# Optimization experiments

Measured on AMD Instinct MI355X. Metric: run time of the kernel, lower is better.

Reference implementation:

```python
import jax, jax.numpy as jnp
import numpy as np

H = 8   # num_heads
D = 64  # out_features per head

def setup_inputs() -> dict:
    key = jax.random.key(0)
    k1, k2, k3, k4 = jax.random.split(key, 4)
    B, N, F_IN, E = 2, 8192, 512, 65536
    x = jax.random.normal(k1, (B, N, F_IN), dtype=jnp.float32)
    edge_indices = jax.random.randint(k2, (2, E), 0, N)
    W = jax.random.normal(k3, (H * D, F_IN), dtype=jnp.float32) * (1.0 / np.sqrt(F_IN))
    a = jax.random.normal(k4, (2 * D, 1), dtype=jnp.float32) * 0.1
    return {"x": x, "edge_indices": edge_indices, "W": W, "a": a}

def reference(x, edge_indices, W, a):
    # Faithful translation of GraphAttentionLayer.forward (eval mode: dropout = identity).
    B, N, _ = x.shape
    h = (x @ W.T).reshape(B, N, H, D)              # [B,N,H,D]
    src, dst = edge_indices[0], edge_indices[1]
    E = src.shape[0]
    h_src = h[:, src]                               # [B,E,H,D]
    h_dst = h[:, dst]                               # [B,E,H,D]
    # cat([h_src,h_dst]) @ a  ==  h_src @ a[:D] + h_dst @ a[D:]
    a1, a2 = a[:D, 0], a[D:, 0]
    scores = jnp.einsum('behd,d->beh', h_src, a1) + jnp.einsum('behd,d->beh', h_dst, a2)
    scores = jax.nn.leaky_relu(scores, negative_slope=0.2)      # [B,E,H]
    # NOTE: original code softmaxes over the BATCH dim (dim=0) per edge.
    sm = jax.nn.softmax(scores, axis=0)                          # [B,E,H]
    last_edge = jnp.full((N,), -1, dtype=jnp.int32).at[src].max(
        jnp.arange(E, dtype=jnp.int32))                          # [N]
    has_edge = last_edge >= 0
    w = jnp.where(has_edge[None, :, None],
                  sm[:, jnp.clip(last_edge, 0)], 0.0)            # [B,N,H]
    # aggregated[:, s] += w[:, s, :, None] * h_dst[:, e] for each edge e with src[e]==s
    # (weights fully built before aggregation loop) => w[s] * segment_sum(h_dst over src)
    agg_dst = jnp.zeros((B, N, H, D), dtype=h.dtype).at[:, src].add(h_dst)
    aggregated = w[..., None] * agg_dst                          # [B,N,H,D]
    return aggregated.mean(axis=2)                               # [B,N,D]
```

## Files before the change

kernel.cpp:

```cpp
#include <hip/hip_runtime.h>
#include <stdint.h>

#define H_HEADS 8
#define DDIM 64
#define NNODES 8192
#define BB 2
#define FIN 512
#define FOUT 512
#define EDGES 65536
#define CAP 32

typedef unsigned short u16;
typedef unsigned int u32;
typedef __bf16 bf16x8 __attribute__((ext_vector_type(8)));
typedef float f32x4 __attribute__((ext_vector_type(4)));

__device__ __forceinline__ u16 f2bf(float f) {
    u32 u = __float_as_uint(f);
    return (u16)((u + 0x7FFFu + ((u >> 16) & 1u)) >> 16);
}
__device__ __forceinline__ float bf2f(u32 s) {
    return __uint_as_float(s << 16);
}
__device__ __forceinline__ uint4 pack8(float4 a, float4 b) {
    return make_uint4(f2bf(a.x) | ((u32)f2bf(a.y) << 16),
                      f2bf(a.z) | ((u32)f2bf(a.w) << 16),
                      f2bf(b.x) | ((u32)f2bf(b.y) << 16),
                      f2bf(b.z) | ((u32)f2bf(b.w) << 16));
}

#define NWB (FOUT * FIN / 8 / 256)
#define NEB 64
__global__ __launch_bounds__(256) void prep_kernel(
    const float* __restrict__ W, const int* __restrict__ src,
    const int* __restrict__ dst, u16* __restrict__ Wb,
    int* __restrict__ cursor, int* __restrict__ le_pack,
    int* __restrict__ csr_dst) {
    int blk = blockIdx.x;
    if (blk < NWB) {
        int i = blk * 256 + threadIdx.x;
        const float4* p = (const float4*)W;
        float4 v0 = p[(size_t)i * 2], v1 = p[(size_t)i * 2 + 1];
        ((uint4*)Wb)[i] = pack8(v0, v1);
    } else {
        int t = (blk - NWB) * 256 + threadIdx.x;
#pragma unroll
        for (int k = 0; k < 4; k++) {
            int e = t * 4 + k;
            int s = src[e], d = dst[e];
            int slot = atomicAdd(&cursor[s], 1);
            if (slot < CAP) csr_dst[(size_t)s * CAP + slot] = d;
            atomicMax(&le_pack[s], (e << 13) | d);
        }
    }
}

#define GLDS(g, l)                                                              \
    __builtin_amdgcn_global_load_lds(                                           \
        (const __attribute__((address_space(1))) u32*)(g),                      \
        (__attribute__((address_space(3))) u32*)(l), 16, 0, 0)

__global__ __launch_bounds__(256) void gemm_mfma(const float* __restrict__ X,
                                                 const u16* __restrict__ Bm,
                                                 const float* __restrict__ a,
                                                 u16* __restrict__ C,
                                                 float* __restrict__ s1,
                                                 float* __restrict__ s2) {
    __shared__ u16 As[128 * 32];
    __shared__ u16 Bs[128 * 32];
    int tid = threadIdx.x;
    int gb = blockIdx.x;
    int m_idx = (gb & 7) | ((gb >> 5) << 3);
    int n_idx = (gb >> 3) & 3;
    int m0 = m_idx * 128, n0 = n_idx * 128;
    int lane = tid & 63, wv = tid >> 6;
    int wr = (wv >> 1) * 64, wc = (wv & 1) * 64;
    int l15 = lane & 15, quad = lane >> 4;
    f32x4 acc[4][4] = {};

    float a1v[4], a2v[4];
#pragma unroll
    for (int j = 0; j < 4; j++) {
        a1v[j] = a[j * 16 + l15];
        a2v[j] = a[DDIM + j * 16 + l15];
    }

    int srow = tid >> 2;
    int scol = (tid & 3) * 8;
    const float* Ag = X + (size_t)(m0 + srow) * FIN + scol;
    const u16* Bg = Bm + (size_t)(n0 + srow) * FIN + scol;
    u16* Al = As + tid * 8;
    u16* Bl = Bs + tid * 8;

    for (int k0 = 0; k0 < FIN; k0 += 32) {
        __syncthreads();
        GLDS(Bg + k0, Bl);
        GLDS(Bg + k0 + (size_t)64 * FIN, Bl + 64 * 32);
        float4 fa0 = *(const float4*)(Ag + k0);
        float4 fa1 = *(const float4*)(Ag + k0 + 4);
        float4 fb0 = *(const float4*)(Ag + k0 + (size_t)64 * FIN);
        float4 fb1 = *(const float4*)(Ag + k0 + (size_t)64 * FIN + 4);
        *(uint4*)Al = pack8(fa0, fa1);
        *(uint4*)(Al + 64 * 32) = pack8(fb0, fb1);
        __syncthreads();
        bf16x8 af[4], bfr[4];
#pragma unroll
        for (int i = 0; i < 4; i++)
            af[i] = *(const bf16x8*)(As + (wr + i * 16 + l15) * 32 + quad * 8);
#pragma unroll
        for (int j = 0; j < 4; j++)
            bfr[j] = *(const bf16x8*)(Bs + (wc + j * 16 + l15) * 32 + quad * 8);
#pragma unroll
        for (int i = 0; i < 4; i++)
#pragma unroll
            for (int j = 0; j < 4; j++)
                acc[i][j] = __builtin_amdgcn_mfma_f32_16x16x32_bf16(
                    af[i], bfr[j], acc[i][j], 0, 0, 0);
    }

#pragma unroll
    for (int i = 0; i < 4; i++) {
        int row_base = m0 + wr + i * 16 + quad * 4;
#pragma unroll
        for (int j = 0; j < 4; j++) {
            int col = n0 + wc + j * 16 + l15;
#pragma unroll
            for (int r = 0; r < 4; r++)
                C[(size_t)(row_base + r) * FOUT + col] = f2bf(acc[i][j][r]);
        }
    }

    int head = n_idx * 2 + (wv & 1);
#pragma unroll
    for (int i = 0; i < 4; i++) {
#pragma unroll
        for (int r = 0; r < 4; r++) {
            float p1 = 0.f, p2 = 0.f;
#pragma unroll
            for (int j = 0; j < 4; j++) {
                p1 += a1v[j] * acc[i][j][r];
                p2 += a2v[j] * acc[i][j][r];
            }
#pragma unroll
            for (int m = 1; m <= 8; m <<= 1) {
                p1 += __shfl_xor(p1, m);
                p2 += __shfl_xor(p2, m);
            }
            if (l15 == 0) {
                int row = m0 + wr + i * 16 + quad * 4 + r;
                s1[row * H_HEADS + head] = p1;
                s2[row * H_HEADS + head] = p2;
            }
        }
    }
}

__global__ __launch_bounds__(256) void aggregate(const u16* __restrict__ h,
                                                 const float* __restrict__ s1,
                                                 const float* __restrict__ s2,
                                                 const int* __restrict__ cursor,
                                                 const int* __restrict__ le_pack,
                                                 const int* __restrict__ csr_dst,
                                                 float* __restrict__ out, int N) {
    int n = blockIdx.x * 2 + (threadIdx.x >> 7);
    int b = (threadIdx.x >> 6) & 1;
    int lane = threadIdx.x & 63;
    int head = lane >> 3;

    int deg = cursor[n];
    deg = deg < CAP ? deg : CAP;
    int pk = le_pack[n];

    const int* cp = csr_dst + (size_t)n * CAP;
    int myidx = (lane < CAP) ? cp[lane] : 0;

    float wgt = 0.f;
    if (deg > 0) {
        int dl = pk & 8191;
        float sc0 = s1[(0 * N + n) * H_HEADS + head] +
                    s2[((size_t)0 * N + dl) * H_HEADS + head];
        float sc1 = s1[((size_t)1 * N + n) * H_HEADS + head] +
                    s2[((size_t)1 * N + dl) * H_HEADS + head];
        sc0 = sc0 >= 0.f ? sc0 : 0.2f * sc0;
        sc1 = sc1 >= 0.f ? sc1 : 0.2f * sc1;
        float m = fmaxf(sc0, sc1);
        float e0 = __expf(sc0 - m), e1 = __expf(sc1 - m);
        wgt = (b == 0 ? e0 : e1) / (e0 + e1);
    }

    float acc[8] = {};
    const u16* hb = h + (size_t)b * N * FOUT + lane * 8;
    for (int j0 = 0; j0 < deg; j0 += 4) {
#pragma unroll
        for (int k = 0; k < 4; k++) {
            int j = j0 + k;
            float f = (j < deg) ? 1.0f : 0.0f;
            int dn = (j < deg) ? __shfl(myidx, j) : 0;
            uint4 v = *(const uint4*)(hb + (size_t)dn * FOUT);
            acc[0] = fmaf(f, bf2f(v.x & 0xffffu), acc[0]);
            acc[1] = fmaf(f, bf2f(v.x >> 16), acc[1]);
            acc[2] = fmaf(f, bf2f(v.y & 0xffffu), acc[2]);
            acc[3] = fmaf(f, bf2f(v.y >> 16), acc[3]);
            acc[4] = fmaf(f, bf2f(v.z & 0xffffu), acc[4]);
            acc[5] = fmaf(f, bf2f(v.z >> 16), acc[5]);
            acc[6] = fmaf(f, bf2f(v.w & 0xffffu), acc[6]);
            acc[7] = fmaf(f, bf2f(v.w >> 16), acc[7]);
        }
    }
    float val[8];
#pragma unroll
    for (int k = 0; k < 8; k++) val[k] = acc[k] * wgt;
#pragma unroll
    for (int m = 8; m <= 32; m <<= 1)
#pragma unroll
        for (int k = 0; k < 8; k++) val[k] += __shfl_xor(val[k], m);
    if (lane < 8) {
        float* op = out + ((size_t)b * N + n) * DDIM + lane * 8;
        const float inv = 1.0f / H_HEADS;
        *(float4*)op = make_float4(val[0] * inv, val[1] * inv, val[2] * inv,
                                   val[3] * inv);
        *(float4*)(op + 4) = make_float4(val[4] * inv, val[5] * inv,
                                         val[6] * inv, val[7] * inv);
    }
}

extern "C" void kernel_launch(void* const* d_in, const int* in_sizes, int n_in,
                              void* d_out, int out_size, void* d_ws,
                              size_t ws_size, hipStream_t stream) {
    const float* x = (const float*)d_in[0];
    const int* edges = (const int*)d_in[1];
    const float* W = (const float*)d_in[2];
    const float* a = (const float*)d_in[3];
    float* out = (float*)d_out;

    const int* src = edges;
    const int* dst = edges + EDGES;

    char* p = (char*)d_ws;
    auto carve = [&](size_t bytes) {
        char* r = p;
        p += (bytes + 255) & ~(size_t)255;
        return r;
    };
    u16* Wb = (u16*)carve((size_t)FOUT * FIN * 2);
    u16* h = (u16*)carve((size_t)BB * NNODES * FOUT * 2);
    float* s1 = (float*)carve((size_t)BB * NNODES * H_HEADS * 4);
    float* s2 = (float*)carve((size_t)BB * NNODES * H_HEADS * 4);
    int* cursor = (int*)carve(NNODES * 4);
    int* le_pack = (int*)carve(NNODES * 4);
    int* csr_dst = (int*)carve((size_t)NNODES * CAP * 4);

    const int M = BB * NNODES;

    hipMemsetAsync(cursor, 0, 2 * NNODES * 4, stream);
    prep_kernel<<<NWB + NEB, 256, 0, stream>>>(W, src, dst, Wb, cursor,
                                               le_pack, csr_dst);
    gemm_mfma<<<(M / 128) * (FOUT / 128), 256, 0, stream>>>(x, Wb, a, h, s1,
                                                            s2);
    aggregate<<<NNODES / 2, 256, 0, stream>>>(h, s1, s2, cursor, le_pack,
                                              csr_dst, out, NNODES);
}
```

Baseline: 125.0 us.

## Pre-convert X to bf16 in prep kernel and async-load both GEMM operands

The fp32-to-bf16 conversion of X moves out of the GEMM inner loop into the prep kernel, so the GEMM can stream both A and B tiles with global_load_lds straight into shared memory. This removes the register round-trip and repeated conversion of X, since each X tile is reread by the four N-column blocks. In exchange it adds an extra 16 MB bf16 write and read pass over X in a separate kernel. The aggregate loop is also split into a full-group-of-four body and a scalar tail, dropping the masked FMAs.

```diff
diff --git a/kernel.cpp b/kernel.cpp
--- a/kernel.cpp
+++ b/kernel.cpp
@@ -29,21 +29,18 @@
                       f2bf(b.z) | ((u32)f2bf(b.w) << 16));
 }
 
+#define NEB 64
 #define NWB (FOUT * FIN / 8 / 256)
-#define NEB 64
+#define NXB (BB * NNODES * FIN / 8 / 256)
 __global__ __launch_bounds__(256) void prep_kernel(
-    const float* __restrict__ W, const int* __restrict__ src,
-    const int* __restrict__ dst, u16* __restrict__ Wb,
+    const float* __restrict__ W, const float* __restrict__ X,
+    const int* __restrict__ src, const int* __restrict__ dst,
+    u16* __restrict__ Wb, u16* __restrict__ Xb,
     int* __restrict__ cursor, int* __restrict__ le_pack,
     int* __restrict__ csr_dst) {
     int blk = blockIdx.x;
-    if (blk < NWB) {
-        int i = blk * 256 + threadIdx.x;
-        const float4* p = (const float4*)W;
-        float4 v0 = p[(size_t)i * 2], v1 = p[(size_t)i * 2 + 1];
-        ((uint4*)Wb)[i] = pack8(v0, v1);
-    } else {
-        int t = (blk - NWB) * 256 + threadIdx.x;
+    if (blk < NEB) {
+        int t = blk * 256 + threadIdx.x;
 #pragma unroll
         for (int k = 0; k < 4; k++) {
             int e = t * 4 + k;
@@ -52,6 +49,16 @@
             if (slot < CAP) csr_dst[(size_t)s * CAP + slot] = d;
             atomicMax(&le_pack[s], (e << 13) | d);
         }
+    } else if (blk < NEB + NWB) {
+        int i = (blk - NEB) * 256 + threadIdx.x;
+        const float4* p = (const float4*)W;
+        float4 v0 = p[(size_t)i * 2], v1 = p[(size_t)i * 2 + 1];
+        ((uint4*)Wb)[i] = pack8(v0, v1);
+    } else {
+        int i = (blk - NEB - NWB) * 256 + threadIdx.x;
+        const float4* p = (const float4*)X;
+        float4 v0 = p[(size_t)i * 2], v1 = p[(size_t)i * 2 + 1];
+        ((uint4*)Xb)[i] = pack8(v0, v1);
     }
 }
 
@@ -60,7 +67,7 @@
         (const __attribute__((address_space(1))) u32*)(g),                      \
         (__attribute__((address_space(3))) u32*)(l), 16, 0, 0)
 
-__global__ __launch_bounds__(256) void gemm_mfma(const float* __restrict__ X,
+__global__ __launch_bounds__(256) void gemm_mfma(const u16* __restrict__ Am,
                                                  const u16* __restrict__ Bm,
                                                  const float* __restrict__ a,
                                                  u16* __restrict__ C,
@@ -87,21 +94,17 @@
 
     int srow = tid >> 2;
     int scol = (tid & 3) * 8;
-    const float* Ag = X + (size_t)(m0 + srow) * FIN + scol;
+    const u16* Ag = Am + (size_t)(m0 + srow) * FIN + scol;
     const u16* Bg = Bm + (size_t)(n0 + srow) * FIN + scol;
     u16* Al = As + tid * 8;
     u16* Bl = Bs + tid * 8;
 
     for (int k0 = 0; k0 < FIN; k0 += 32) {
         __syncthreads();
+        GLDS(Ag + k0, Al);
+        GLDS(Ag + k0 + (size_t)64 * FIN, Al + 64 * 32);
         GLDS(Bg + k0, Bl);
         GLDS(Bg + k0 + (size_t)64 * FIN, Bl + 64 * 32);
-        float4 fa0 = *(const float4*)(Ag + k0);
-        float4 fa1 = *(const float4*)(Ag + k0 + 4);
-        float4 fb0 = *(const float4*)(Ag + k0 + (size_t)64 * FIN);
-        float4 fb1 = *(const float4*)(Ag + k0 + (size_t)64 * FIN + 4);
-        *(uint4*)Al = pack8(fa0, fa1);
-        *(uint4*)(Al + 64 * 32) = pack8(fb0, fb1);
         __syncthreads();
         bf16x8 af[4], bfr[4];
 #pragma unroll
@@ -153,6 +156,17 @@
             }
         }
     }
+}
+
+__device__ __forceinline__ void acc8(float* acc, uint4 v) {
+    acc[0] += bf2f(v.x & 0xffffu);
+    acc[1] += bf2f(v.x >> 16);
+    acc[2] += bf2f(v.y & 0xffffu);
+    acc[3] += bf2f(v.y >> 16);
+    acc[4] += bf2f(v.z & 0xffffu);
+    acc[5] += bf2f(v.z >> 16);
+    acc[6] += bf2f(v.w & 0xffffu);
+    acc[7] += bf2f(v.w >> 16);
 }
 
 __global__ __launch_bounds__(256) void aggregate(const u16* __restrict__ h,
@@ -190,23 +204,27 @@
 
     float acc[8] = {};
     const u16* hb = h + (size_t)b * N * FOUT + lane * 8;
-    for (int j0 = 0; j0 < deg; j0 += 4) {
-#pragma unroll
-        for (int k = 0; k < 4; k++) {
-            int j = j0 + k;
-            float f = (j < deg) ? 1.0f : 0.0f;
-            int dn = (j < deg) ? __shfl(myidx, j) : 0;
-            uint4 v = *(const uint4*)(hb + (size_t)dn * FOUT);
-            acc[0] = fmaf(f, bf2f(v.x & 0xffffu), acc[0]);
-            acc[1] = fmaf(f, bf2f(v.x >> 16), acc[1]);
-            acc[2] = fmaf(f, bf2f(v.y & 0xffffu), acc[2]);
-            acc[3] = fmaf(f, bf2f(v.y >> 16), acc[3]);
-            acc[4] = fmaf(f, bf2f(v.z & 0xffffu), acc[4]);
-            acc[5] = fmaf(f, bf2f(v.z >> 16), acc[5]);
-            acc[6] = fmaf(f, bf2f(v.w & 0xffffu), acc[6]);
-            acc[7] = fmaf(f, bf2f(v.w >> 16), acc[7]);
-        }
-    }
+    int degm = deg & ~3;
+    for (int j0 = 0; j0 < degm; j0 += 4) {
+        int d0 = __shfl(myidx, j0);
+        int d1 = __shfl(myidx, j0 + 1);
+        int d2 = __shfl(myidx, j0 + 2);
+        int d3 = __shfl(myidx, j0 + 3);
+        uint4 v0 = *(const uint4*)(hb + (size_t)d0 * FOUT);
+        uint4 v1 = *(const uint4*)(hb + (size_t)d1 * FOUT);
+        uint4 v2 = *(const uint4*)(hb + (size_t)d2 * FOUT);
+        uint4 v3 = *(const uint4*)(hb + (size_t)d3 * FOUT);
+        acc8(acc, v0);
+        acc8(acc, v1);
+        acc8(acc, v2);
+        acc8(acc, v3);
+    }
+    for (int j = degm; j < deg; j++) {
+        int dn = __shfl(myidx, j);
+        uint4 v = *(const uint4*)(hb + (size_t)dn * FOUT);
+        acc8(acc, v);
+    }
+
     float val[8];
 #pragma unroll
     for (int k = 0; k < 8; k++) val[k] = acc[k] * wgt;
@@ -243,6 +261,7 @@
         return r;
     };
     u16* Wb = (u16*)carve((size_t)FOUT * FIN * 2);
+    u16* Xb = (u16*)carve((size_t)BB * NNODES * FIN * 2);
     u16* h = (u16*)carve((size_t)BB * NNODES * FOUT * 2);
     float* s1 = (float*)carve((size_t)BB * NNODES * H_HEADS * 4);
     float* s2 = (float*)carve((size_t)BB * NNODES * H_HEADS * 4);
@@ -253,9 +272,9 @@
     const int M = BB * NNODES;
 
     hipMemsetAsync(cursor, 0, 2 * NNODES * 4, stream);
-    prep_kernel<<<NWB + NEB, 256, 0, stream>>>(W, src, dst, Wb, cursor,
-                                               le_pack, csr_dst);
-    gemm_mfma<<<(M / 128) * (FOUT / 128), 256, 0, stream>>>(x, Wb, a, h, s1,
+    prep_kernel<<<NEB + NWB + NXB, 256, 0, stream>>>(W, x, src, dst, Wb, Xb,
+                                                     cursor, le_pack, csr_dst);
+    gemm_mfma<<<(M / 128) * (FOUT / 128), 256, 0, stream>>>(Xb, Wb, a, h, s1,
                                                             s2);
     aggregate<<<NNODES / 2, 256, 0, stream>>>(h, s1, s2, cursor, le_pack,
                                               csr_dst, out, NNODES);
```

Measured after the change: 126.3 us. No clear change (+1.1%).
